# Kernel tuning notes

Hardware: AMD Instinct MI355X
Metric: run time of the kernel (lower is better)

The kernel has to match this reference:

```python
import jax, jax.numpy as jnp
import numpy as np

N = 4096
F_IN = 3000
F_OUT = 64
NEG_INF = jnp.float32(-9e15)


def _xavier(key, shape):
    fan_in, fan_out = shape[0], shape[-1]
    limit = (6.0 / (fan_in + fan_out)) ** 0.5
    return jax.random.uniform(key, shape, jnp.float32, -limit, limit)


def setup_inputs() -> dict:
    key = jax.random.key(0)
    ks = jax.random.split(key, 20)
    feat = jax.random.normal(ks[0], (N, F_IN), jnp.float32)
    feat_a = jax.random.normal(ks[1], (N, F_IN), jnp.float32)
    eye = jnp.eye(N, dtype=jnp.float32)
    adj = jnp.maximum((jax.random.uniform(ks[2], (N, N)) < 0.008).astype(jnp.float32), eye)
    graph_neigh = jnp.maximum((jax.random.uniform(ks[3], (N, N)) < 0.008).astype(jnp.float32), eye)
    return {
        "feat": feat,
        "feat_a": feat_a,
        "adj": adj,
        "graph_neigh": graph_neigh,
        "weight1": _xavier(ks[4], (F_IN, F_OUT)),
        "weight2": _xavier(ks[5], (F_OUT, F_IN)),
        "att_W": _xavier(ks[6], (F_OUT, F_OUT)),
        "a_src": _xavier(ks[7], (F_OUT, 1)),
        "a_dst": _xavier(ks[8], (F_OUT, 1)),
        "mlp_W1": _xavier(ks[9], (F_OUT, 256)),
        "mlp_b1": jnp.zeros((256,), jnp.float32),
        "mlp_W2": _xavier(ks[10], (256, 128)),
        "mlp_b2": jnp.zeros((128,), jnp.float32),
        "mlp_W3": _xavier(ks[11], (128, F_OUT)),
        "mlp_b3": jnp.zeros((F_OUT,), jnp.float32),
        "dmlp_W1": _xavier(ks[12], (F_OUT, 128)),
        "dmlp_b1": jnp.zeros((128,), jnp.float32),
        "dmlp_W2": _xavier(ks[13], (128, F_OUT)),
        "dmlp_b2": jnp.zeros((F_OUT,), jnp.float32),
        "bil_W": _xavier(ks[14], (F_OUT, F_OUT)),
        "bil_b": jnp.zeros((1,), jnp.float32),
    }


def reference(feat, feat_a, adj, graph_neigh,
              weight1, weight2, att_W, a_src, a_dst,
              mlp_W1, mlp_b1, mlp_W2, mlp_b2, mlp_W3, mlp_b3,
              dmlp_W1, dmlp_b1, dmlp_W2, dmlp_b2, bil_W, bil_b):
    relu = jax.nn.relu

    def attention(h):
        Wh = h @ att_W                      # [N, F_OUT]
        e = Wh @ a_src + (Wh @ a_dst).T     # [N, N]
        e = jnp.where(e > 0, e, 0.2 * e)    # LeakyReLU(0.2)
        e = jnp.where(adj > 0, e, NEG_INF)  # mask non-edges
        return jax.nn.softmax(e, axis=1) @ Wh

    def mlp(x):
        x = relu(x @ mlp_W1 + mlp_b1)
        x = relu(x @ mlp_W2 + mlp_b2)
        return x @ mlp_W3 + mlp_b3

    def dmlp(x):  # discriminator MLP: n_h -> 128 -> n_h
        return relu(x @ dmlp_W1 + dmlp_b1) @ dmlp_W2 + dmlp_b2

    def readout(emb):  # AvgReadout + L2 normalize
        g = (graph_neigh @ emb) / jnp.sum(graph_neigh, axis=1, keepdims=True)
        return g / jnp.maximum(jnp.linalg.norm(g, axis=1, keepdims=True), 1e-12)

    def bilinear(x, y):  # nn.Bilinear(n_h, n_h, 1)
        return (jnp.einsum('ni,ij,nj->n', x, bil_W, y) + bil_b)[:, None]

    def disc(c, h_pl, h_mi):
        c, h_pl, h_mi = dmlp(c), dmlp(h_pl), dmlp(h_mi)
        return jnp.concatenate([bilinear(h_pl, c), bilinear(h_mi, c)], axis=1)

    z = mlp(attention(feat @ weight1))
    hiden_emb = z
    h = adj @ (z @ weight2)                 # spmm(adj, z @ weight2)
    emb = relu(z)
    z_a = mlp(attention(feat_a @ weight1))
    emb_a = relu(z_a)
    g = jax.nn.sigmoid(readout(emb))
    g_a = jax.nn.sigmoid(readout(emb_a))
    ret = disc(g, emb, emb_a)
    ret_a = disc(g_a, emb_a, emb)
    return (hiden_emb, h, ret, ret_a)
```

## Files before the change

kernel.cpp:

```cpp
#include <hip/hip_runtime.h>

#define NN   4096
#define FIN  3000
#define MAXN 128

typedef unsigned short u16;
typedef __bf16 bf16x8 __attribute__((ext_vector_type(8)));
typedef float f32x16 __attribute__((ext_vector_type(16)));

__device__ __forceinline__ float bf2f(u16 u) { union { unsigned int i; float f; } v; v.i = ((unsigned int)u) << 16; return v.f; }
__device__ __forceinline__ u16 f2bf(float f) {
    union { float f; unsigned int i; } v; v.f = f;
    return (u16)((v.i + 0x7FFFu + ((v.i >> 16) & 1u)) >> 16);
}
__device__ __forceinline__ bf16x8 bzero8() {
    union { unsigned long long q[2]; bf16x8 v; } u; u.q[0] = 0ull; u.q[1] = 0ull; return u.v;
}
__device__ __forceinline__ f32x16 fzero16() {
    f32x16 v;
    #pragma unroll
    for (int i = 0; i < 16; i++) v[i] = 0.f;
    return v;
}

__global__ __launch_bounds__(1024) void k_detect(const u16* __restrict__ feat, int* __restrict__ flag)
{
    __shared__ int tot;
    if (threadIdx.x == 0) tot = 0;
    __syncthreads();
    int ins = 0;
    for (int i = threadIdx.x; i < 16384; i += 1024) {
        u16 u = feat[i];
        int e = (u >> 7) & 0xFF;
        if (u != 0 && (e < 90 || e > 160)) ins++;
    }
    atomicAdd(&tot, ins);
    __syncthreads();
    if (threadIdx.x == 0) *flag = (tot > 1024) ? 1 : 0;
}

__global__ __launch_bounds__(256) void k_convw(const int* __restrict__ flag,
    const void* s0, const void* s1, const void* s2, const void* s3,
    const void* s4, const void* s5, const void* s6, const void* s7,
    const void* s8, const void* s9, const void* s10, const void* s11,
    const void* s12, const void* s13, const void* s14, const void* s15,
    float* __restrict__ dst)
{
    const void* srcs[16] = {s0,s1,s2,s3,s4,s5,s6,s7,s8,s9,s10,s11,s12,s13,s14,s15};
    const int offs[16] = {0,192000,196096,196160,196224,212608,212864,245632,245760,253952,254016,262208,262336,270528,270592,274688};
    const int ns[16]   = {192000,4096,64,64,16384,256,32768,128,8192,64,8192,128,8192,64,4096,1};
    int seg = blockIdx.y;
    int i = blockIdx.x * 256 + threadIdx.x;
    if (i >= ns[seg]) return;
    float v = (*flag) ? ((const float*)srcs[seg])[i] : bf2f(((const u16*)srcs[seg])[i]);
    dst[offs[seg] + i] = v;
}

__global__ __launch_bounds__(256) void k_convw2(const int* __restrict__ flag,
    const void* __restrict__ src, float* __restrict__ dst)
{
    int i = blockIdx.x * 256 + threadIdx.x;
    if (i >= 192000) return;
    dst[i] = (*flag) ? ((const float*)src)[i] : bf2f(((const u16*)src)[i]);
}

__global__ __launch_bounds__(256) void k_convw1t(const int* __restrict__ flag,
    const void* __restrict__ w1src, u16* __restrict__ BtH, u16* __restrict__ BtL)
{
    int i = blockIdx.x * 256 + threadIdx.x;
    if (i >= 64 * 3008) return;
    int c = i / 3008, k = i - c * 3008;
    float v = 0.f;
    if (k < 3000)
        v = (*flag) ? ((const float*)w1src)[(size_t)k * 64 + c]
                    : bf2f(((const u16*)w1src)[(size_t)k * 64 + c]);
    u16 h = f2bf(v);
    float r = v - bf2f(h);
    BtH[(size_t)c * 3008 + k] = h;
    BtL[(size_t)c * 3008 + k] = f2bf(r);
}

__global__ __launch_bounds__(256) void k_build_csr(const int* __restrict__ flag,
    const void* __restrict__ Av, const void* __restrict__ Gv,
    int* __restrict__ aCnt, int* __restrict__ aIdx,
    int* __restrict__ gCnt, int* __restrict__ gIdx)
{
    bool isf = (*flag != 0);
    const void* M = blockIdx.y ? Gv : Av;
    int* cnt = blockIdx.y ? gCnt : aCnt;
    int* idx = blockIdx.y ? gIdx : aIdx;
    int row = blockIdx.x, t = threadIdx.x;
    int c0 = t * 16;
    unsigned int mask = 0; int my = 0;
    if (isf) {
        const float* r = (const float*)M + (size_t)row * NN + c0;
        #pragma unroll
        for (int j = 0; j < 16; j++) if (r[j] != 0.f) { mask |= 1u << j; my++; }
    } else {
        const u16* r = (const u16*)M + (size_t)row * NN + c0;
        #pragma unroll
        for (int j = 0; j < 16; j++) if (r[j] != 0) { mask |= 1u << j; my++; }
    }
    __shared__ int sc[256];
    sc[t] = my;
    __syncthreads();
    for (int d = 1; d < 256; d <<= 1) {
        int v = (t >= d) ? sc[t - d] : 0;
        __syncthreads();
        sc[t] += v;
        __syncthreads();
    }
    int pos = sc[t] - my;
    for (int j = 0; j < 16; j++) {
        if (mask & (1u << j)) {
            if (pos < MAXN) idx[(size_t)row * MAXN + pos] = c0 + j;
            pos++;
        }
    }
    if (t == 0) { int total = sc[255]; cnt[row] = (total < MAXN) ? total : MAXN; }
}

__global__ __launch_bounds__(512) void k_featgemm_mfma(const int* __restrict__ flag,
    const void* __restrict__ F0v, const void* __restrict__ F1v,
    const u16* __restrict__ BtH, float* __restrict__ X0, float* __restrict__ X1)
{
    if (*flag) return;
    const u16* F = (const u16*)(blockIdx.y ? F1v : F0v);
    float* X = blockIdx.y ? X1 : X0;
    int r0 = blockIdx.x * 32;
    int tid = threadIdx.x;
    int w  = tid >> 6;
    int l  = tid & 63;
    int lr = l & 31;
    int kg = l >> 5;
    const u16* arow = F   + (size_t)(r0 + lr) * FIN + kg * 8;
    const u16* b0p  = BtH + (size_t)lr * 3008 + kg * 8;
    const u16* b1p  = BtH + (size_t)(lr + 32) * 3008 + kg * 8;
    f32x16 acc0 = fzero16(), acc1 = fzero16();
    #pragma unroll 4
    for (int s = w; s < 188; s += 8) {
        int kk = s * 16;
        bf16x8 a;
        if (kk + kg * 8 < FIN) a = *(const bf16x8*)(arow + kk);
        else                   a = bzero8();
        bf16x8 b0 = *(const bf16x8*)(b0p + kk);
        bf16x8 b1 = *(const bf16x8*)(b1p + kk);
        acc0 = __builtin_amdgcn_mfma_f32_32x32x16_bf16(a, b0, acc0, 0, 0, 0);
        acc1 = __builtin_amdgcn_mfma_f32_32x32x16_bf16(a, b1, acc1, 0, 0, 0);
    }
    __shared__ float red[8][2048];
    float* rp = red[w];
    #pragma unroll
    for (int reg = 0; reg < 16; reg++) {
        int row = (reg & 3) + 8 * (reg >> 2) + 4 * kg;
        rp[row * 64 + lr] = acc0[reg];
    }
    #pragma unroll
    for (int reg = 0; reg < 16; reg++) {
        int row = (reg & 3) + 8 * (reg >> 2) + 4 * kg;
        rp[row * 64 + 32 + lr] = acc1[reg];
    }
    __syncthreads();
    for (int i = tid; i < 2048; i += 512) {
        float s0 = 0.f;
        #pragma unroll
        for (int j = 0; j < 8; j++) s0 += red[j][i];
        X[(size_t)r0 * 64 + i] = s0;
    }
}

__global__ __launch_bounds__(512) void k_featgemm_mfma_f32(const int* __restrict__ flag,
    const void* __restrict__ F0v, const void* __restrict__ F1v,
    const u16* __restrict__ BtH, const u16* __restrict__ BtL,
    float* __restrict__ X0, float* __restrict__ X1)
{
    if (!*flag) return;
    const float* F = (const float*)(blockIdx.y ? F1v : F0v);
    float* X = blockIdx.y ? X1 : X0;
    int r0 = blockIdx.x * 32;
    int tid = threadIdx.x;
    int w  = tid >> 6;
    int l  = tid & 63;
    int lr = l & 31;
    int kg = l >> 5;
    const float* arow = F + (size_t)(r0 + lr) * FIN + kg * 8;
    const u16* b0h = BtH + (size_t)lr * 3008 + kg * 8;
    const u16* b1h = BtH + (size_t)(lr + 32) * 3008 + kg * 8;
    const u16* b0l = BtL + (size_t)lr * 3008 + kg * 8;
    const u16* b1l = BtL + (size_t)(lr + 32) * 3008 + kg * 8;
    f32x16 acc0 = fzero16(), acc1 = fzero16();
    #pragma unroll 2
    for (int s = w; s < 188; s += 8) {
        int kk = s * 16;
        float av[8];
        if (kk + kg * 8 < FIN) {
            float4 p0 = *(const float4*)(arow + kk);
            float4 p1 = *(const float4*)(arow + kk + 4);
            av[0] = p0.x; av[1] = p0.y; av[2] = p0.z; av[3] = p0.w;
            av[4] = p1.x; av[5] = p1.y; av[6] = p1.z; av[7] = p1.w;
        } else {
            #pragma unroll
            for (int j = 0; j < 8; j++) av[j] = 0.f;
        }
        bf16x8 ah, al;
        #pragma unroll
        for (int j = 0; j < 8; j++) {
            __bf16 hv = (__bf16)av[j];
            float  rv = av[j] - (float)hv;
            ah[j] = hv;
            al[j] = (__bf16)rv;
        }
        bf16x8 v0h = *(const bf16x8*)(b0h + kk);
        bf16x8 v1h = *(const bf16x8*)(b1h + kk);
        bf16x8 v0l = *(const bf16x8*)(b0l + kk);
        bf16x8 v1l = *(const bf16x8*)(b1l + kk);
        acc0 = __builtin_amdgcn_mfma_f32_32x32x16_bf16(ah, v0h, acc0, 0, 0, 0);
        acc0 = __builtin_amdgcn_mfma_f32_32x32x16_bf16(al, v0h, acc0, 0, 0, 0);
        acc0 = __builtin_amdgcn_mfma_f32_32x32x16_bf16(ah, v0l, acc0, 0, 0, 0);
        acc1 = __builtin_amdgcn_mfma_f32_32x32x16_bf16(ah, v1h, acc1, 0, 0, 0);
        acc1 = __builtin_amdgcn_mfma_f32_32x32x16_bf16(al, v1h, acc1, 0, 0, 0);
        acc1 = __builtin_amdgcn_mfma_f32_32x32x16_bf16(ah, v1l, acc1, 0, 0, 0);
    }
    __shared__ float red[8][2048];
    float* rp = red[w];
    #pragma unroll
    for (int reg = 0; reg < 16; reg++) {
        int row = (reg & 3) + 8 * (reg >> 2) + 4 * kg;
        rp[row * 64 + lr] = acc0[reg];
    }
    #pragma unroll
    for (int reg = 0; reg < 16; reg++) {
        int row = (reg & 3) + 8 * (reg >> 2) + 4 * kg;
        rp[row * 64 + 32 + lr] = acc1[reg];
    }
    __syncthreads();
    for (int i = tid; i < 2048; i += 512) {
        float s0 = 0.f;
        #pragma unroll
        for (int j = 0; j < 8; j++) s0 += red[j][i];
        X[(size_t)r0 * 64 + i] = s0;
    }
}

__global__ __launch_bounds__(64) void k_whsd(
    const float* __restrict__ X1, const float* __restrict__ X2,
    const float* __restrict__ AW, const float* __restrict__ asrc, const float* __restrict__ adst,
    float* __restrict__ Wh1, float* __restrict__ Wh2,
    float* __restrict__ s1, float* __restrict__ s2,
    float* __restrict__ d1, float* __restrict__ d2)
{
    const float* X = blockIdx.y ? X2 : X1;
    float* Wh = blockIdx.y ? Wh2 : Wh1;
    float* sv = blockIdx.y ? s2 : s1;
    float* dv = blockIdx.y ? d2 : d1;
    int row = blockIdx.x, c = threadIdx.x;
    __shared__ float x[64];
    x[c] = X[(size_t)row * 64 + c];
    __syncthreads();
    float acc = 0.f;
    #pragma unroll 16
    for (int k = 0; k < 64; k++) acc += x[k] * AW[k * 64 + c];
    Wh[(size_t)row * 64 + c] = acc;
    float vs = acc * asrc[c];
    float vd = acc * adst[c];
    #pragma unroll
    for (int off = 32; off > 0; off >>= 1) { vs += __shfl_down(vs, off); vd += __shfl_down(vd, off); }
    if (c == 0) { sv[row] = vs; dv[row] = vd; }
}

__global__ __launch_bounds__(128) void k_attn(
    const int* __restrict__ cnt, const int* __restrict__ idx,
    const float* __restrict__ s1, const float* __restrict__ s2,
    const float* __restrict__ d1, const float* __restrict__ d2,
    const float* __restrict__ Wh1, const float* __restrict__ Wh2,
    float* __restrict__ A1, float* __restrict__ A2)
{
    const float* sp = blockIdx.y ? s2 : s1;
    const float* dp = blockIdx.y ? d2 : d1;
    const float* Wh = blockIdx.y ? Wh2 : Wh1;
    float* A = blockIdx.y ? A2 : A1;
    int row = blockIdx.x, tid = threadIdx.x;
    int n = cnt[row];
    __shared__ int js[MAXN];
    __shared__ float ps[MAXN];
    __shared__ float red2[2];
    __shared__ float ared[2][64];
    for (int k = tid; k < n; k += 128) js[k] = idx[(size_t)row * MAXN + k];
    __syncthreads();
    float si = sp[row];
    float m = -3.0e38f;
    for (int k = tid; k < n; k += 128) {
        float e = si + dp[js[k]];
        e = e > 0.f ? e : 0.2f * e;
        ps[k] = e;
        m = fmaxf(m, e);
    }
    #pragma unroll
    for (int off = 32; off > 0; off >>= 1) m = fmaxf(m, __shfl_down(m, off));
    if ((tid & 63) == 0) red2[tid >> 6] = m;
    __syncthreads();
    m = fmaxf(red2[0], red2[1]);
    __syncthreads();
    float zz = 0.f;
    for (int k = tid; k < n; k += 128) {
        float p = __expf(ps[k] - m);
        ps[k] = p;
        zz += p;
    }
    #pragma unroll
    for (int off = 32; off > 0; off >>= 1) zz += __shfl_down(zz, off);
    if ((tid & 63) == 0) red2[tid >> 6] = zz;
    __syncthreads();
    float Z = red2[0] + red2[1];
    Z = fmaxf(Z, 1e-20f);
    int f = tid & 63, half = tid >> 6;
    float acc = 0.f;
    for (int k = half; k < n; k += 2) acc += ps[k] * Wh[(size_t)js[k] * 64 + f];
    ared[half][f] = acc;
    __syncthreads();
    if (tid < 64) A[(size_t)row * 64 + f] = (ared[0][f] + ared[1][f]) / Z;
}

__global__ __launch_bounds__(256) void k_mlp(const int* __restrict__ flag,
    const float* __restrict__ A1, const float* __restrict__ A2,
    const float* __restrict__ W1, const float* __restrict__ b1,
    const float* __restrict__ W2, const float* __restrict__ b2,
    const float* __restrict__ W3, const float* __restrict__ b3,
    float* __restrict__ Z1, float* __restrict__ Z2, void* __restrict__ hidenv)
{
    const float* A = blockIdx.y ? A2 : A1;
    float* Z = blockIdx.y ? Z2 : Z1;
    int row0 = blockIdx.x * 4, tid = threadIdx.x;
    __shared__ float x[4][64], h1[4][256], h2[4][128];
    {
        int r = tid >> 6, c = tid & 63;
        x[r][c] = A[(size_t)(row0 + r) * 64 + c];
    }
    __syncthreads();
    {
        float a0 = b1[tid], a1v = a0, a2v = a0, a3v = a0;
        #pragma unroll 8
        for (int k = 0; k < 64; k++) {
            float w = W1[k * 256 + tid];
            a0 += x[0][k] * w; a1v += x[1][k] * w; a2v += x[2][k] * w; a3v += x[3][k] * w;
        }
        h1[0][tid] = fmaxf(a0, 0.f);  h1[1][tid] = fmaxf(a1v, 0.f);
        h1[2][tid] = fmaxf(a2v, 0.f); h1[3][tid] = fmaxf(a3v, 0.f);
    }
    __syncthreads();
    if (tid < 128) {
        float a0 = b2[tid], a1v = a0, a2v = a0, a3v = a0;
        #pragma unroll 8
        for (int k = 0; k < 256; k++) {
            float w = W2[k * 128 + tid];
            a0 += h1[0][k] * w; a1v += h1[1][k] * w; a2v += h1[2][k] * w; a3v += h1[3][k] * w;
        }
        h2[0][tid] = fmaxf(a0, 0.f);  h2[1][tid] = fmaxf(a1v, 0.f);
        h2[2][tid] = fmaxf(a2v, 0.f); h2[3][tid] = fmaxf(a3v, 0.f);
    }
    __syncthreads();
    if (tid < 64) {
        float a[4];
        a[0] = a[1] = a[2] = a[3] = b3[tid];
        #pragma unroll 8
        for (int k = 0; k < 128; k++) {
            float w = W3[k * 64 + tid];
            a[0] += h2[0][k] * w; a[1] += h2[1][k] * w; a[2] += h2[2][k] * w; a[3] += h2[3][k] * w;
        }
        bool isf = (*flag != 0);
        #pragma unroll
        for (int r = 0; r < 4; r++) {
            size_t ei = (size_t)(row0 + r) * 64 + tid;
            Z[ei] = a[r];
            if (blockIdx.y == 0) {
                if (isf) ((float*)hidenv)[ei] = a[r];
                else     ((u16*)hidenv)[ei] = f2bf(a[r]);
            }
        }
    }
}

__global__ __launch_bounds__(64) void k_spmm(
    const int* __restrict__ cnt, const int* __restrict__ idx,
    const float* __restrict__ Z, float* __restrict__ T)
{
    int row = blockIdx.x, f = threadIdx.x;
    int n = cnt[row];
    const int* ir = idx + (size_t)row * MAXN;
    float acc = 0.f;
    for (int k = 0; k < n; k++) acc += Z[(size_t)ir[k] * 64 + f];
    T[(size_t)row * 64 + f] = acc;
}

__global__ __launch_bounds__(256) void k_hgemm(const int* __restrict__ flag,
    const float* __restrict__ T, const float* __restrict__ W2f, void* __restrict__ outv)
{
    bool isf = (*flag != 0);
    int r0 = blockIdx.x * 8, tid = threadIdx.x;
    __shared__ float tt[8][64];
    for (int i = tid; i < 512; i += 256) tt[i >> 6][i & 63] = T[(size_t)r0 * 64 + i];
    __syncthreads();
    for (int c = tid; c < FIN; c += 256) {
        float a[8] = {0,0,0,0,0,0,0,0};
        #pragma unroll 8
        for (int k = 0; k < 64; k++) {
            float w = W2f[(size_t)k * FIN + c];
            #pragma unroll
            for (int i = 0; i < 8; i++) a[i] += tt[i][k] * w;
        }
        #pragma unroll
        for (int i = 0; i < 8; i++) {
            size_t ei = 262144 + (size_t)(r0 + i) * FIN + c;
            if (isf) ((float*)outv)[ei] = a[i];
            else     ((u16*)outv)[ei] = f2bf(a[i]);
        }
    }
}

__global__ __launch_bounds__(64) void k_readout(
    const int* __restrict__ cnt, const int* __restrict__ idx,
    const float* __restrict__ Z1, const float* __restrict__ Z2,
    float* __restrict__ G1, float* __restrict__ G2)
{
    const float* Z = blockIdx.y ? Z2 : Z1;
    float* G = blockIdx.y ? G2 : G1;
    int row = blockIdx.x, f = threadIdx.x;
    int n = cnt[row];
    const int* ir = idx + (size_t)row * MAXN;
    float acc = 0.f;
    for (int k = 0; k < n; k++) acc += fmaxf(Z[(size_t)ir[k] * 64 + f], 0.f);
    acc /= (float)(n > 0 ? n : 1);
    float sq = acc * acc;
    #pragma unroll
    for (int off = 32; off > 0; off >>= 1) sq += __shfl_down(sq, off);
    sq = __shfl(sq, 0);
    float nrm = fmaxf(sqrtf(sq), 1e-12f);
    float v = acc / nrm;
    G[(size_t)row * 64 + f] = 1.f / (1.f + __expf(-v));
}

__global__ __launch_bounds__(128) void k_dmlp(
    const float* __restrict__ z, const float* __restrict__ za,
    const float* __restrict__ g, const float* __restrict__ ga,
    const float* __restrict__ W1, const float* __restrict__ b1,
    const float* __restrict__ W2, const float* __restrict__ b2,
    float* __restrict__ De, float* __restrict__ Dea,
    float* __restrict__ Dg, float* __restrict__ Dga)
{
    int w = blockIdx.y;
    const float* X = (w == 0) ? z : (w == 1) ? za : (w == 2) ? g : ga;
    float* O = (w == 0) ? De : (w == 1) ? Dea : (w == 2) ? Dg : Dga;
    int doRelu = (w < 2);
    int row0 = blockIdx.x * 4, tid = threadIdx.x;
    __shared__ float x[4][64], h1[4][128];
    for (int i = tid; i < 256; i += 128) {
        int r = i >> 6, c = i & 63;
        float v = X[(size_t)(row0 + r) * 64 + c];
        x[r][c] = doRelu ? fmaxf(v, 0.f) : v;
    }
    __syncthreads();
    {
        float a0 = b1[tid], a1v = a0, a2v = a0, a3v = a0;
        #pragma unroll 8
        for (int k = 0; k < 64; k++) {
            float w_ = W1[k * 128 + tid];
            a0 += x[0][k] * w_; a1v += x[1][k] * w_; a2v += x[2][k] * w_; a3v += x[3][k] * w_;
        }
        h1[0][tid] = fmaxf(a0, 0.f);  h1[1][tid] = fmaxf(a1v, 0.f);
        h1[2][tid] = fmaxf(a2v, 0.f); h1[3][tid] = fmaxf(a3v, 0.f);
    }
    __syncthreads();
    if (tid < 64) {
        float a[4];
        a[0] = a[1] = a[2] = a[3] = b2[tid];
        #pragma unroll 8
        for (int k = 0; k < 128; k++) {
            float w_ = W2[k * 64 + tid];
            a[0] += h1[0][k] * w_; a[1] += h1[1][k] * w_; a[2] += h1[2][k] * w_; a[3] += h1[3][k] * w_;
        }
        #pragma unroll
        for (int r = 0; r < 4; r++) O[(size_t)(row0 + r) * 64 + tid] = a[r];
    }
}

__global__ __launch_bounds__(64) void k_bilin(const int* __restrict__ flag,
    const float* __restrict__ De, const float* __restrict__ Dea,
    const float* __restrict__ Dg, const float* __restrict__ Dga,
    const float* __restrict__ BW, const float* __restrict__ bb, void* __restrict__ outv)
{
    int w = blockIdx.y;
    const float* X = (w == 0 || w == 3) ? De : Dea;
    const float* Y = (w <= 1) ? Dg : Dga;
    size_t bse = (w <= 1) ? (size_t)12550144 : (size_t)12558336;
    int col = (w == 0 || w == 2) ? 0 : 1;
    int row = blockIdx.x, k = threadIdx.x;
    __shared__ float x[64], y[64];
    x[k] = X[(size_t)row * 64 + k];
    y[k] = Y[(size_t)row * 64 + k];
    __syncthreads();
    float wv = 0.f;
    #pragma unroll 8
    for (int j = 0; j < 64; j++) wv += BW[k * 64 + j] * y[j];
    float v = x[k] * wv;
    #pragma unroll
    for (int off = 32; off > 0; off >>= 1) v += __shfl_down(v, off);
    if (k == 0) {
        float r = v + bb[0];
        size_t ei = bse + (size_t)row * 2 + col;
        if (*flag) ((float*)outv)[ei] = r;
        else       ((u16*)outv)[ei] = f2bf(r);
    }
}

extern "C" void kernel_launch(void* const* d_in, const int* in_sizes, int n_in,
                              void* d_out, int out_size, void* d_ws, size_t ws_size,
                              hipStream_t stream) {
    const void* feat   = d_in[0];
    const void* feat_a = d_in[1];
    const void* adj    = d_in[2];
    const void* gn     = d_in[3];
    const void* w1     = d_in[4];
    const void* w2     = d_in[5];
    const void* attW   = d_in[6];
    const void* a_src  = d_in[7];
    const void* a_dst  = d_in[8];
    const void* mW1    = d_in[9];
    const void* mb1    = d_in[10];
    const void* mW2    = d_in[11];
    const void* mb2    = d_in[12];
    const void* mW3    = d_in[13];
    const void* mb3    = d_in[14];
    const void* dW1    = d_in[15];
    const void* db1    = d_in[16];
    const void* dW2    = d_in[17];
    const void* db2    = d_in[18];
    const void* bW     = d_in[19];
    const void* bb     = d_in[20];
    (void)in_sizes; (void)n_in; (void)out_size;

    char* wsb = (char*)d_ws;
    int*   flag = (int*)wsb;
    float* T    = (float*)(wsb + 256);
    float* w2f  = (float*)(wsb + 256 + 1048576);
    (void)ws_size;

    char* sc = (char*)d_out + 1048576;
    size_t soff = 0;
    auto salloc = [&](size_t nbytes) -> void* {
        void* p = (void*)(sc + soff);
        soff += (nbytes + 255) & ~(size_t)255;
        return p;
    };
    const size_t NV = (size_t)NN * 64;
    float* wA   = (float*)salloc((size_t)274689 * 4);
    int*   aCnt = (int*)salloc(NN * 4);
    int*   gCnt = (int*)salloc(NN * 4);
    int*   aIdx = (int*)salloc((size_t)NN * MAXN * 4);
    int*   gIdx = (int*)salloc((size_t)NN * MAXN * 4);
    float* X1  = (float*)salloc(NV * 4);
    float* X2  = (float*)salloc(NV * 4);
    float* Wh1 = (float*)salloc(NV * 4);
    float* Wh2 = (float*)salloc(NV * 4);
    float* A1  = (float*)salloc(NV * 4);
    float* A2  = (float*)salloc(NV * 4);
    float* z   = (float*)salloc(NV * 4);
    float* za  = (float*)salloc(NV * 4);
    float* g   = (float*)salloc(NV * 4);
    float* ga  = (float*)salloc(NV * 4);
    float* De  = (float*)salloc(NV * 4);
    float* Dea = (float*)salloc(NV * 4);
    float* Dg  = (float*)salloc(NV * 4);
    float* Dga = (float*)salloc(NV * 4);
    float* s1  = (float*)salloc(NN * 4);
    float* s2  = (float*)salloc(NN * 4);
    float* d1  = (float*)salloc(NN * 4);
    float* d2  = (float*)salloc(NN * 4);

    float* w1f   = wA + 0;
    float* attWf = wA + 192000;
    float* asrcf = wA + 196096;
    float* adstf = wA + 196160;
    float* mW1f  = wA + 196224;
    float* mb1f  = wA + 212608;
    float* mW2f  = wA + 212864;
    float* mb2f  = wA + 245632;
    float* mW3f  = wA + 245760;
    float* mb3f  = wA + 253952;
    float* dW1f  = wA + 254016;
    float* db1f  = wA + 262208;
    float* dW2f  = wA + 262336;
    float* db2f  = wA + 270528;
    float* bWf   = wA + 270592;
    float* bbf   = wA + 274688;

    u16* BtH = (u16*)De;
    u16* BtL = (u16*)Dea;

    k_detect<<<1, 1024, 0, stream>>>((const u16*)feat, flag);
    k_convw<<<dim3(750, 16), 256, 0, stream>>>(flag,
        w1, attW, a_src, a_dst, mW1, mb1, mW2, mb2, mW3, mb3,
        dW1, db1, dW2, db2, bW, bb, wA);
    k_convw2<<<750, 256, 0, stream>>>(flag, w2, w2f);
    k_convw1t<<<752, 256, 0, stream>>>(flag, w1, BtH, BtL);
    k_build_csr<<<dim3(NN, 2), 256, 0, stream>>>(flag, adj, gn, aCnt, aIdx, gCnt, gIdx);
    k_featgemm_mfma<<<dim3(NN / 32, 2), 512, 0, stream>>>(flag, feat, feat_a, BtH, X1, X2);
    k_featgemm_mfma_f32<<<dim3(NN / 32, 2), 512, 0, stream>>>(flag, feat, feat_a, BtH, BtL, X1, X2);
    k_whsd<<<dim3(NN, 2), 64, 0, stream>>>(X1, X2, attWf, asrcf, adstf, Wh1, Wh2, s1, s2, d1, d2);
    k_attn<<<dim3(NN, 2), 128, 0, stream>>>(aCnt, aIdx, s1, s2, d1, d2, Wh1, Wh2, A1, A2);
    k_mlp<<<dim3(NN / 4, 2), 256, 0, stream>>>(flag, A1, A2, mW1f, mb1f, mW2f, mb2f, mW3f, mb3f, z, za, d_out);
    k_readout<<<dim3(NN, 2), 64, 0, stream>>>(gCnt, gIdx, z, za, g, ga);
    k_dmlp<<<dim3(NN / 4, 4), 128, 0, stream>>>(z, za, g, ga, dW1f, db1f, dW2f, db2f, De, Dea, Dg, Dga);
    k_bilin<<<dim3(NN, 4), 64, 0, stream>>>(flag, De, Dea, Dg, Dga, bWf, bbf, d_out);
    k_spmm<<<NN, 64, 0, stream>>>(aCnt, aIdx, z, T);
    k_hgemm<<<512, 256, 0, stream>>>(flag, T, w2f, d_out);
}
```

Measured before the change: 493.9 us.

## Use split-bf16 MFMA for output GEMM and split-K the feature GEMM

Replaces the scalar FP32 h-GEMM (T @ weight2) with a 3-pass split-bf16 MFMA kernel that reads a transposed hi/lo bf16 copy of weight2 built in the prep kernel. The FP32-input feature GEMM is also split along K across two blocks that combine through atomicAdd into zeroed outputs, which adds blocks for better occupancy. This adds a memset and atomic traffic, and makes the summation order nondeterministic.

```diff
diff --git a/kernel.cpp b/kernel.cpp
--- a/kernel.cpp
+++ b/kernel.cpp
@@ -56,12 +56,20 @@
     dst[offs[seg] + i] = v;
 }
 
-__global__ __launch_bounds__(256) void k_convw2(const int* __restrict__ flag,
-    const void* __restrict__ src, float* __restrict__ dst)
+__global__ __launch_bounds__(256) void k_convw2t(const int* __restrict__ flag,
+    const void* __restrict__ src, u16* __restrict__ WH, u16* __restrict__ WL)
 {
     int i = blockIdx.x * 256 + threadIdx.x;
-    if (i >= 192000) return;
-    dst[i] = (*flag) ? ((const float*)src)[i] : bf2f(((const u16*)src)[i]);
+    if (i >= 3008 * 64) return;
+    int n = i >> 6, k = i & 63;
+    float v = 0.f;
+    if (n < FIN)
+        v = (*flag) ? ((const float*)src)[(size_t)k * FIN + n]
+                    : bf2f(((const u16*)src)[(size_t)k * FIN + n]);
+    u16 h = f2bf(v);
+    float r = v - bf2f(h);
+    WH[i] = h;
+    WL[i] = f2bf(r);
 }
 
 __global__ __launch_bounds__(256) void k_convw1t(const int* __restrict__ flag,
@@ -183,6 +191,7 @@
     int l  = tid & 63;
     int lr = l & 31;
     int kg = l >> 5;
+    int s0 = blockIdx.z * 8 + w;
     const float* arow = F + (size_t)(r0 + lr) * FIN + kg * 8;
     const u16* b0h = BtH + (size_t)lr * 3008 + kg * 8;
     const u16* b1h = BtH + (size_t)(lr + 32) * 3008 + kg * 8;
@@ -190,7 +199,7 @@
     const u16* b1l = BtL + (size_t)(lr + 32) * 3008 + kg * 8;
     f32x16 acc0 = fzero16(), acc1 = fzero16();
     #pragma unroll 2
-    for (int s = w; s < 188; s += 8) {
+    for (int s = s0; s < 188; s += 16) {
         int kk = s * 16;
         float av[8];
         if (kk + kg * 8 < FIN) {
@@ -235,10 +244,10 @@
     }
     __syncthreads();
     for (int i = tid; i < 2048; i += 512) {
-        float s0 = 0.f;
-        #pragma unroll
-        for (int j = 0; j < 8; j++) s0 += red[j][i];
-        X[(size_t)r0 * 64 + i] = s0;
+        float s0s = 0.f;
+        #pragma unroll
+        for (int j = 0; j < 8; j++) s0s += red[j][i];
+        atomicAdd(&X[(size_t)r0 * 64 + i], s0s);
     }
 }
 
@@ -392,27 +401,50 @@
     T[(size_t)row * 64 + f] = acc;
 }
 
-__global__ __launch_bounds__(256) void k_hgemm(const int* __restrict__ flag,
-    const float* __restrict__ T, const float* __restrict__ W2f, void* __restrict__ outv)
+__global__ __launch_bounds__(256) void k_hgemm_mfma(const int* __restrict__ flag,
+    const float* __restrict__ T, const u16* __restrict__ WH, const u16* __restrict__ WL,
+    void* __restrict__ outv)
 {
     bool isf = (*flag != 0);
-    int r0 = blockIdx.x * 8, tid = threadIdx.x;
-    __shared__ float tt[8][64];
-    for (int i = tid; i < 512; i += 256) tt[i >> 6][i & 63] = T[(size_t)r0 * 64 + i];
-    __syncthreads();
-    for (int c = tid; c < FIN; c += 256) {
-        float a[8] = {0,0,0,0,0,0,0,0};
-        #pragma unroll 8
-        for (int k = 0; k < 64; k++) {
-            float w = W2f[(size_t)k * FIN + c];
-            #pragma unroll
-            for (int i = 0; i < 8; i++) a[i] += tt[i][k] * w;
-        }
-        #pragma unroll
-        for (int i = 0; i < 8; i++) {
-            size_t ei = 262144 + (size_t)(r0 + i) * FIN + c;
-            if (isf) ((float*)outv)[ei] = a[i];
-            else     ((u16*)outv)[ei] = f2bf(a[i]);
+    int tid = threadIdx.x;
+    int w = tid >> 6, l = tid & 63, lr = l & 31, kg = l >> 5;
+    int ct = blockIdx.y * 4 + w;
+    if (ct >= 94) return;
+    int r0 = blockIdx.x * 32, c0 = ct * 32;
+    const float* tp = T + (size_t)(r0 + lr) * 64 + kg * 8;
+    bf16x8 ah[4], al[4];
+    #pragma unroll
+    for (int s = 0; s < 4; s++) {
+        float4 p0 = *(const float4*)(tp + s * 16);
+        float4 p1 = *(const float4*)(tp + s * 16 + 4);
+        float av[8] = {p0.x, p0.y, p0.z, p0.w, p1.x, p1.y, p1.z, p1.w};
+        #pragma unroll
+        for (int j = 0; j < 8; j++) {
+            __bf16 hv = (__bf16)av[j];
+            ah[s][j] = hv;
+            al[s][j] = (__bf16)(av[j] - (float)hv);
+        }
+    }
+    const u16* bh = WH + (size_t)(c0 + lr) * 64 + kg * 8;
+    const u16* bl = WL + (size_t)(c0 + lr) * 64 + kg * 8;
+    f32x16 acc = fzero16();
+    #pragma unroll
+    for (int s = 0; s < 4; s++) {
+        bf16x8 vh = *(const bf16x8*)(bh + s * 16);
+        bf16x8 vl = *(const bf16x8*)(bl + s * 16);
+        acc = __builtin_amdgcn_mfma_f32_32x32x16_bf16(ah[s], vh, acc, 0, 0, 0);
+        acc = __builtin_amdgcn_mfma_f32_32x32x16_bf16(al[s], vh, acc, 0, 0, 0);
+        acc = __builtin_amdgcn_mfma_f32_32x32x16_bf16(ah[s], vl, acc, 0, 0, 0);
+    }
+    int col = c0 + lr;
+    bool cok = col < FIN;
+    #pragma unroll
+    for (int reg = 0; reg < 16; reg++) {
+        int row = (reg & 3) + 8 * (reg >> 2) + 4 * kg;
+        size_t ei = 262144 + (size_t)(r0 + row) * FIN + col;
+        if (cok) {
+            if (isf) ((float*)outv)[ei] = acc[reg];
+            else     ((u16*)outv)[ei] = f2bf(acc[reg]);
         }
     }
 }
@@ -541,7 +573,8 @@
     char* wsb = (char*)d_ws;
     int*   flag = (int*)wsb;
     float* T    = (float*)(wsb + 256);
-    float* w2f  = (float*)(wsb + 256 + 1048576);
+    u16*   W2tH = (u16*)(wsb + 256 + 1048576);
+    u16*   W2tL = W2tH + 3008 * 64;
     (void)ws_size;
 
     char* sc = (char*)d_out + 1048576;
@@ -600,11 +633,12 @@
     k_convw<<<dim3(750, 16), 256, 0, stream>>>(flag,
         w1, attW, a_src, a_dst, mW1, mb1, mW2, mb2, mW3, mb3,
         dW1, db1, dW2, db2, bW, bb, wA);
-    k_convw2<<<750, 256, 0, stream>>>(flag, w2, w2f);
+    k_convw2t<<<752, 256, 0, stream>>>(flag, w2, W2tH, W2tL);
     k_convw1t<<<752, 256, 0, stream>>>(flag, w1, BtH, BtL);
     k_build_csr<<<dim3(NN, 2), 256, 0, stream>>>(flag, adj, gn, aCnt, aIdx, gCnt, gIdx);
+    hipMemsetAsync(X1, 0, 2 * NV * 4, stream);
     k_featgemm_mfma<<<dim3(NN / 32, 2), 512, 0, stream>>>(flag, feat, feat_a, BtH, X1, X2);
-    k_featgemm_mfma_f32<<<dim3(NN / 32, 2), 512, 0, stream>>>(flag, feat, feat_a, BtH, BtL, X1, X2);
+    k_featgemm_mfma_f32<<<dim3(NN / 32, 2, 2), 512, 0, stream>>>(flag, feat, feat_a, BtH, BtL, X1, X2);
     k_whsd<<<dim3(NN, 2), 64, 0, stream>>>(X1, X2, attWf, asrcf, adstf, Wh1, Wh2, s1, s2, d1, d2);
     k_attn<<<dim3(NN, 2), 128, 0, stream>>>(aCnt, aIdx, s1, s2, d1, d2, Wh1, Wh2, A1, A2);
     k_mlp<<<dim3(NN / 4, 2), 256, 0, stream>>>(flag, A1, A2, mW1f, mb1f, mW2f, mb2f, mW3f, mb3f, z, za, d_out);
@@ -612,5 +646,5 @@
     k_dmlp<<<dim3(NN / 4, 4), 128, 0, stream>>>(z, za, g, ga, dW1f, db1f, dW2f, db2f, De, Dea, Dg, Dga);
     k_bilin<<<dim3(NN, 4), 64, 0, stream>>>(flag, De, Dea, Dg, Dga, bWf, bbf, d_out);
     k_spmm<<<NN, 64, 0, stream>>>(aCnt, aIdx, z, T);
-    k_hgemm<<<512, 256, 0, stream>>>(flag, T, w2f, d_out);
-}
+    k_hgemm_mfma<<<dim3(NN / 32, 24), 256, 0, stream>>>(flag, T, W2tH, W2tL, d_out);
+}
```

After: 471.2 us. 1.05x faster.
